# Optimization experiments

Measured on AMD Instinct MI355X. Metric: run time of the kernel, lower is better.

The kernel has to match this reference:

```python
import jax, jax.numpy as jnp
import numpy as np

N, E = 20000, 256000
NODE_DIM, EDGE_DIM = 128, 8
HID, HEADS, LAYERS = 64, 4, 3   # TransformerConv: out_channels per head = HID, concat=False
CLASSES, GRAPHS = 3, 64
HC = HEADS * HID


def setup_inputs() -> dict:
    key = jax.random.key(0)
    ks = iter(jax.random.split(key, 40))
    g = lambda shape, s=0.05: jax.random.normal(next(ks), shape, dtype=jnp.float32) * s
    z = lambda shape: jnp.zeros(shape, jnp.float32)
    return dict(
        x=jax.random.normal(next(ks), (N, NODE_DIM), dtype=jnp.float32),
        edge_attr=jax.random.normal(next(ks), (E, EDGE_DIM), dtype=jnp.float32),
        node_W=g((NODE_DIM, HID)), node_b=z((HID,)),
        e1_W=g((EDGE_DIM, HID)), e1_b=z((HID,)),
        e2_W=g((HID, HID)), e2_b=z((HID,)),
        Wq=g((LAYERS, HID, HC)), bq=z((LAYERS, HC)),
        Wk=g((LAYERS, HID, HC)), bk=z((LAYERS, HC)),
        Wv=g((LAYERS, HID, HC)), bv=z((LAYERS, HC)),
        We=g((LAYERS, HID, HC)),                      # lin_edge has bias=False in PyG
        Wskip=g((LAYERS, HID, HID)), bskip=z((LAYERS, HID)),
        ln_g=jnp.ones((LAYERS, HID), jnp.float32), ln_b=z((LAYERS, HID)),
        cls_W=g((HID, CLASSES)), cls_b=z((CLASSES,)),
        edge_index=jax.random.randint(next(ks), (2, E), 0, N),
        batch=jnp.sort(jax.random.randint(next(ks), (N,), 0, GRAPHS)),
    )


def _layer_norm(x, g, b, eps=1e-5):
    m = x.mean(-1, keepdims=True)
    v = x.var(-1, keepdims=True)
    return (x - m) * jax.lax.rsqrt(v + eps) * g + b


def reference(x, edge_attr, node_W, node_b, e1_W, e1_b, e2_W, e2_b,
              Wq, bq, Wk, bk, Wv, bv, We, Wskip, bskip, ln_g, ln_b,
              cls_W, cls_b, edge_index, batch):
    src, dst = edge_index[0], edge_index[1]          # messages flow src -> dst
    h = x @ node_W + node_b                          # [N, HID]
    e = jax.nn.relu(edge_attr @ e1_W + e1_b) @ e2_W + e2_b  # [E, HID]
    scale = 1.0 / jnp.sqrt(jnp.float32(HID))
    for l in range(LAYERS):                          # fixed small layer count
        res = h
        q = (h @ Wq[l] + bq[l]).reshape(N, HEADS, HID)
        k = (h @ Wk[l] + bk[l]).reshape(N, HEADS, HID)
        v = (h @ Wv[l] + bv[l]).reshape(N, HEADS, HID)
        ee = (e @ We[l]).reshape(E, HEADS, HID)      # per-layer edge projection
        kj = k[src] + ee                             # [E, H, C] irregular gather
        alpha = (q[dst] * kj).sum(-1) * scale        # [E, H]
        amax = jax.ops.segment_max(alpha, dst, num_segments=N)
        ea = jnp.exp(alpha - amax[dst])
        denom = jax.ops.segment_sum(ea, dst, num_segments=N)
        alpha = ea / denom[dst]                      # segment softmax over in-edges
        # dropout on alpha: identity in eval mode
        msg = (v[src] + ee) * alpha[..., None]       # [E, H, C]
        agg = jax.ops.segment_sum(msg, dst, num_segments=N)  # [N, H, C]
        conv = agg.mean(axis=1) + (res @ Wskip[l] + bskip[l])  # concat=False, root_weight
        h = jax.nn.relu(_layer_norm(conv + res, ln_g[l], ln_b[l]))
        # model-level dropout: identity in eval mode
    gsum = jax.ops.segment_sum(h, batch, num_segments=GRAPHS)
    gcnt = jax.ops.segment_sum(jnp.ones((N, 1), h.dtype), batch, num_segments=GRAPHS)
    pooled = gsum / jnp.maximum(gcnt, 1.0)           # global mean pool
    return jax.nn.log_softmax(pooled @ cls_W + cls_b, axis=-1)  # [GRAPHS, CLASSES]
```

## Files before the change

kernel.cpp:

```cpp
#include <hip/hip_runtime.h>
#include <hip/hip_bf16.h>
#include <math.h>

#define NN 20000
#define NE 256000
#define NODE_DIM_ 128
#define EDGE_DIM_ 8
#define HID 64
#define HEADS 4
#define NLAYERS 3
#define NCLASSES 3
#define NGRAPHS 64
#define HC 256
#define NPB 8
#define EB 64
#define EPB 16

typedef __hip_bfloat16 bf16;

__device__ __forceinline__ float B2F(bf16 x) { return __bfloat162float(x); }
__device__ __forceinline__ bf16 F2B(float x) { return __float2bfloat16(x); }
__device__ __forceinline__ float U2F(unsigned short u) { return __uint_as_float(((unsigned)u) << 16); }
__device__ __forceinline__ int clampi(int x, int lo, int hi) { return min(max(x, lo), hi); }

__global__ void gt_write_const(float* out, int n, float val) {
    int i = blockIdx.x * blockDim.x + threadIdx.x;
    if (i < n) out[i] = val;
}

__global__ void gt_zero_i32(int* p, int n) {
    int i = blockIdx.x * blockDim.x + threadIdx.x;
    if (i < n) p[i] = 0;
}

__global__ void gt_transpose_we(const float* __restrict__ We, float* __restrict__ WeT) {
    int idx = blockIdx.x * blockDim.x + threadIdx.x;
    if (idx >= NLAYERS * HID * HC) return;
    int l = idx / (HID * HC);
    int r = idx % (HID * HC);
    int c = r / HC;
    int u = r % HC;
    int hh = u >> 6, j = u & 63;
    WeT[idx] = We[(size_t)l * HID * HC + (size_t)j * HC + hh * 64 + c];
}

__global__ void gt_prep_wcomb(const float* __restrict__ We, const float* __restrict__ Wskip,
                              float* __restrict__ Wc) {
    int idx = blockIdx.x * blockDim.x + threadIdx.x;
    if (idx >= NLAYERS * 320 * 64) return;
    int l = idx / (320 * 64);
    int r = idx % (320 * 64);
    int kk = r / 64;
    int c = r % 64;
    float val;
    if (kk < 256) {
        int hh = kk >> 6, j = kk & 63;
        val = We[(size_t)l * HID * HC + (size_t)j * HC + hh * 64 + c];
    } else {
        int j = kk - 256;
        val = Wskip[(size_t)l * HID * HID + (size_t)j * HID + c];
    }
    Wc[(size_t)l * 320 * 64 + (size_t)((kk >> 2) * 64 + c) * 4 + (kk & 3)] = val;
}

__global__ void gt_node_proj(const float* __restrict__ x, const float* __restrict__ W,
                             const float* __restrict__ b, float* __restrict__ h) {
    int t = threadIdx.x;
    int n = blockIdx.x * 4 + (t >> 6);
    int c = t & 63;
    __shared__ float xr[4][NODE_DIM_];
    for (int i = t; i < 4 * NODE_DIM_; i += 256) {
        int nn = blockIdx.x * 4 + i / NODE_DIM_;
        xr[i / NODE_DIM_][i % NODE_DIM_] = (nn < NN) ? x[(size_t)nn * NODE_DIM_ + i % NODE_DIM_] : 0.f;
    }
    __syncthreads();
    if (n >= NN) return;
    float acc = 0.f;
#pragma unroll 8
    for (int j = 0; j < NODE_DIM_; ++j) acc += xr[t >> 6][j] * W[j * HID + c];
    h[(size_t)n * HID + c] = acc + b[c];
}

__global__ void gt_edge_mlp(const float* __restrict__ ea, const float* __restrict__ W1,
                            const float* __restrict__ b1, const float* __restrict__ W2,
                            const float* __restrict__ b2, bf16* __restrict__ ef) {
    int t = threadIdx.x;
    int c = t & 63, slot = t >> 6;
    int e0 = blockIdx.x * EB;
    __shared__ float aS[EB][EDGE_DIM_];
    __shared__ float t1s[EB][HID];
    for (int i = t; i < EB * EDGE_DIM_; i += 256) {
        ((float*)aS)[i] = ea[(size_t)e0 * EDGE_DIM_ + i];
    }
    float w1r[EDGE_DIM_];
#pragma unroll
    for (int j = 0; j < EDGE_DIM_; ++j) w1r[j] = W1[j * HID + c];
    float b1c = b1[c], b2c = b2[c];
    __syncthreads();
#pragma unroll
    for (int es16 = 0; es16 < 16; ++es16) {
        int es = slot * 16 + es16;
        float acc = b1c;
#pragma unroll
        for (int j = 0; j < EDGE_DIM_; ++j) acc += aS[es][j] * w1r[j];
        t1s[es][c] = fmaxf(acc, 0.f);
    }
    __syncthreads();
    float acc2[16];
#pragma unroll
    for (int i = 0; i < 16; ++i) acc2[i] = b2c;
    for (int j = 0; j < HID; ++j) {
        float w = W2[j * HID + c];
#pragma unroll
        for (int es16 = 0; es16 < 16; ++es16) acc2[es16] += t1s[slot * 16 + es16][j] * w;
    }
#pragma unroll
    for (int es16 = 0; es16 < 16; ++es16) {
        int es = slot * 16 + es16;
        ef[(size_t)(e0 + es) * HID + c] = F2B(acc2[es16]);
    }
}

__global__ void gt_count_dst(const int* __restrict__ ei, int* cnt) {
    int e = blockIdx.x * blockDim.x + threadIdx.x;
    if (e < NE) {
        int d = clampi(ei[NE + e], 0, NN - 1);
        atomicAdd(&cnt[d], 1);
    }
}

__global__ void gt_scan_csr(const int* __restrict__ cnt, int* __restrict__ rp, int* __restrict__ cur) {
    __shared__ int part[256];
    int tid = threadIdx.x;
    const int CH = (NN + 255) / 256;
    int s0 = tid * CH, s1 = min(s0 + CH, NN);
    int s = 0;
    for (int i = s0; i < s1; ++i) s += cnt[i];
    part[tid] = s;
    __syncthreads();
    for (int off = 1; off < 256; off <<= 1) {
        int vv = (tid >= off) ? part[tid - off] : 0;
        __syncthreads();
        if (tid >= off) part[tid] += vv;
        __syncthreads();
    }
    int base = (tid == 0) ? 0 : part[tid - 1];
    for (int i = s0; i < s1; ++i) {
        rp[i] = base;
        cur[i] = base;
        base += cnt[i];
    }
    if (tid == 255) rp[NN] = part[255];
}

__global__ void gt_fill_csr(const int* __restrict__ ei, int* cur, int* csr) {
    int e = blockIdx.x * blockDim.x + threadIdx.x;
    if (e < NE) {
        int d = clampi(ei[NE + e], 0, NN - 1);
        int pos = atomicAdd(&cur[d], 1);
        if (pos >= 0 && pos < NE) csr[pos] = e;
    }
}

__global__ void gt_qkv_qe(const float* __restrict__ h, const float* __restrict__ Wq,
                          const float* __restrict__ bq, const float* __restrict__ Wk,
                          const float* __restrict__ bk, const float* __restrict__ Wv,
                          const float* __restrict__ bv, const float* __restrict__ WeT,
                          float* __restrict__ q, bf16* __restrict__ k, bf16* __restrict__ v,
                          float* __restrict__ qe) {
    int t = threadIdx.x;
    int n0 = blockIdx.x * NPB;
    __shared__ float hs[NPB][HID];
    __shared__ float qs[NPB][HC];
    for (int i = t; i < NPB * HID; i += 256) {
        int nn = n0 + i / HID;
        hs[i / HID][i % HID] = (nn < NN) ? h[(size_t)nn * HID + i % HID] : 0.f;
    }
    __syncthreads();
    float aq[NPB], ak[NPB], av[NPB];
#pragma unroll
    for (int i = 0; i < NPB; ++i) { aq[i] = 0.f; ak[i] = 0.f; av[i] = 0.f; }
    for (int j = 0; j < HID; ++j) {
        float wq = Wq[j * HC + t];
        float wk = Wk[j * HC + t];
        float wv = Wv[j * HC + t];
#pragma unroll
        for (int i = 0; i < NPB; ++i) {
            aq[i] += hs[i][j] * wq;
            ak[i] += hs[i][j] * wk;
            av[i] += hs[i][j] * wv;
        }
    }
    float bqv = bq[t], bkv = bk[t], bvv = bv[t];
    for (int i = 0; i < NPB; ++i) {
        int nn = n0 + i;
        float qr = aq[i] + bqv;
        qs[i][t] = qr;
        if (nn < NN) {
            q[(size_t)nn * HC + t] = qr;
            k[(size_t)nn * HC + t] = F2B(ak[i] + bkv);
            v[(size_t)nn * HC + t] = F2B(av[i] + bvv);
        }
    }
    __syncthreads();
    int h2 = t >> 6;
    float accq[NPB];
#pragma unroll
    for (int i = 0; i < NPB; ++i) accq[i] = 0.f;
    for (int c = 0; c < HID; ++c) {
        float wt = WeT[(size_t)c * HC + t];
#pragma unroll
        for (int i = 0; i < NPB; ++i) accq[i] += qs[i][h2 * 64 + c] * wt;
    }
    for (int i = 0; i < NPB; ++i) {
        int nn = n0 + i;
        if (nn < NN) qe[(size_t)nn * HC + t] = accq[i];
    }
}

__global__ void gt_attn_core(float* __restrict__ q, float* __restrict__ qe,
                             const bf16* __restrict__ k, const bf16* __restrict__ v,
                             const bf16* __restrict__ ef,
                             const int* __restrict__ rp, const int* __restrict__ csr,
                             const int* __restrict__ ei) {
    int t = threadIdx.x;
    int lane = t & 63, wave = t >> 6;
    int n = blockIdx.x * 4 + wave;
    if (n >= NN) return;

    const float4* q4 = (const float4*)q;
    const float4* qe4 = (const float4*)qe;
    const ushort4* k4p = (const ushort4*)k;
    const ushort4* v4p = (const ushort4*)v;
    const ushort4* e4p = (const ushort4*)ef;

    float4 qv = q4[(size_t)n * 64 + lane];
    float4 qev = qe4[(size_t)n * 64 + lane];

    int s0 = clampi(rp[n], 0, NE), s1 = clampi(rp[n + 1], s0, NE);
    float m = -1e30f, lr = 0.f;
    float4 accv = make_float4(0.f, 0.f, 0.f, 0.f);
    float4 accs = make_float4(0.f, 0.f, 0.f, 0.f);

    for (int base = s0; base < s1; base += 64) {
        int cnt = min(64, s1 - base);
        int eL = 0, srcL = 0;
        if (lane < cnt) {
            eL = clampi(csr[base + lane], 0, NE - 1);
            srcL = clampi(ei[eL], 0, NN - 1);
        }
        int e0 = __builtin_amdgcn_readlane(eL, 0);
        int r0 = __builtin_amdgcn_readlane(srcL, 0);
        ushort4 kk = k4p[(size_t)r0 * 64 + lane];
        ushort4 vv = v4p[(size_t)r0 * 64 + lane];
        ushort4 ee = e4p[(size_t)e0 * 16 + (lane & 15)];
        for (int i = 0; i < cnt; ++i) {
            ushort4 kc = kk, vc = vv, ec = ee;
            if (i + 1 < cnt) {
                int e2 = __builtin_amdgcn_readlane(eL, i + 1);
                int r2 = __builtin_amdgcn_readlane(srcL, i + 1);
                kk = k4p[(size_t)r2 * 64 + lane];
                vv = v4p[(size_t)r2 * 64 + lane];
                ee = e4p[(size_t)e2 * 16 + (lane & 15)];
            }
            float p = qv.x * U2F(kc.x) + qv.y * U2F(kc.y) + qv.z * U2F(kc.z) + qv.w * U2F(kc.w)
                    + qev.x * U2F(ec.x) + qev.y * U2F(ec.y) + qev.z * U2F(ec.z) + qev.w * U2F(ec.w);
            p += __shfl_xor(p, 8, 16);
            p += __shfl_xor(p, 4, 16);
            p += __shfl_xor(p, 2, 16);
            p += __shfl_xor(p, 1, 16);
            p *= 0.125f;
            float nm = fmaxf(m, p);
            float sc = __expf(m - nm);
            float wg = __expf(p - nm);
            m = nm;
            lr = lr * sc + wg;
            accv.x = accv.x * sc + wg * U2F(vc.x);
            accv.y = accv.y * sc + wg * U2F(vc.y);
            accv.z = accv.z * sc + wg * U2F(vc.z);
            accv.w = accv.w * sc + wg * U2F(vc.w);
            accs.x = accs.x * sc + wg * U2F(ec.x);
            accs.y = accs.y * sc + wg * U2F(ec.y);
            accs.z = accs.z * sc + wg * U2F(ec.z);
            accs.w = accs.w * sc + wg * U2F(ec.w);
        }
    }
    float inv = (s1 > s0) ? 0.25f / lr : 0.f;
    float4 rs = make_float4(accs.x * inv, accs.y * inv, accs.z * inv, accs.w * inv);
    ((float4*)q)[(size_t)n * 64 + lane] = rs;
    float4 rv = make_float4(accv.x * inv, accv.y * inv, accv.z * inv, accv.w * inv);
    rv.x += __shfl_xor(rv.x, 16, 64); rv.x += __shfl_xor(rv.x, 32, 64);
    rv.y += __shfl_xor(rv.y, 16, 64); rv.y += __shfl_xor(rv.y, 32, 64);
    rv.z += __shfl_xor(rv.z, 16, 64); rv.z += __shfl_xor(rv.z, 32, 64);
    rv.w += __shfl_xor(rv.w, 16, 64); rv.w += __shfl_xor(rv.w, 32, 64);
    if (lane < 16) ((float4*)qe)[(size_t)n * 64 + lane] = rv;
}

__global__ void gt_epilogue(const float* __restrict__ acc_s, const float* __restrict__ acc_vm,
                            const float* __restrict__ Wc, const float* __restrict__ bskip,
                            const float* __restrict__ lng, const float* __restrict__ lnb,
                            float* __restrict__ h) {
    int t = threadIdx.x;
    int c = t & 63, qw = t >> 6;
    int n0 = blockIdx.x * EPB;
    __shared__ float sK[EPB][320];
    __shared__ float sVM[EPB][64];
    const float4* as4 = (const float4*)acc_s;
    for (int i = t; i < EPB * 64; i += 256) {
        int nd = i >> 6, j4 = i & 63;
        *(float4*)&sK[nd][4 * j4] = as4[(size_t)(n0 + nd) * 64 + j4];
    }
    const float4* h4g = (const float4*)h;
    const float4* vm4 = (const float4*)acc_vm;
    for (int i = t; i < EPB * 16; i += 256) {
        int nd = i >> 4, j4 = i & 15;
        *(float4*)&sK[nd][256 + 4 * j4] = h4g[(size_t)(n0 + nd) * 16 + j4];
        *(float4*)&sVM[nd][4 * j4] = vm4[(size_t)(n0 + nd) * 64 + j4];
    }
    __syncthreads();
    int nb = qw * 4;
    const float4* r0 = (const float4*)&sK[nb][0];
    const float4* r1 = (const float4*)&sK[nb + 1][0];
    const float4* r2 = (const float4*)&sK[nb + 2][0];
    const float4* r3 = (const float4*)&sK[nb + 3][0];
    const float4* W4 = (const float4*)Wc;
    float a0 = 0.f, a1 = 0.f, a2 = 0.f, a3 = 0.f;
#pragma unroll 4
    for (int k4 = 0; k4 < 80; ++k4) {
        float4 w = W4[k4 * 64 + c];
        float4 x0 = r0[k4]; a0 += x0.x * w.x + x0.y * w.y + x0.z * w.z + x0.w * w.w;
        float4 x1 = r1[k4]; a1 += x1.x * w.x + x1.y * w.y + x1.z * w.z + x1.w * w.w;
        float4 x2 = r2[k4]; a2 += x2.x * w.x + x2.y * w.y + x2.z * w.z + x2.w * w.w;
        float4 x3 = r3[k4]; a3 += x3.x * w.x + x3.y * w.y + x3.z * w.z + x3.w * w.w;
    }
    float bsk = bskip[c], g = lng[c], bb = lnb[c];
    float y0 = a0 + sVM[nb][c] + sK[nb][256 + c] + bsk;
    float y1 = a1 + sVM[nb + 1][c] + sK[nb + 1][256 + c] + bsk;
    float y2 = a2 + sVM[nb + 2][c] + sK[nb + 2][256 + c] + bsk;
    float y3 = a3 + sVM[nb + 3][c] + sK[nb + 3][256 + c] + bsk;
    float m0 = y0, m1 = y1, m2 = y2, m3 = y3;
#pragma unroll
    for (int s = 32; s > 0; s >>= 1) {
        m0 += __shfl_xor(m0, s, 64);
        m1 += __shfl_xor(m1, s, 64);
        m2 += __shfl_xor(m2, s, 64);
        m3 += __shfl_xor(m3, s, 64);
    }
    m0 *= (1.f / HID); m1 *= (1.f / HID); m2 *= (1.f / HID); m3 *= (1.f / HID);
    float d0 = y0 - m0, d1 = y1 - m1, d2 = y2 - m2, d3 = y3 - m3;
    float v0 = d0 * d0, v1 = d1 * d1, v2 = d2 * d2, v3 = d3 * d3;
#pragma unroll
    for (int s = 32; s > 0; s >>= 1) {
        v0 += __shfl_xor(v0, s, 64);
        v1 += __shfl_xor(v1, s, 64);
        v2 += __shfl_xor(v2, s, 64);
        v3 += __shfl_xor(v3, s, 64);
    }
    v0 *= (1.f / HID); v1 *= (1.f / HID); v2 *= (1.f / HID); v3 *= (1.f / HID);
    h[(size_t)(n0 + nb) * HID + c]     = fmaxf(d0 * rsqrtf(v0 + 1e-5f) * g + bb, 0.f);
    h[(size_t)(n0 + nb + 1) * HID + c] = fmaxf(d1 * rsqrtf(v1 + 1e-5f) * g + bb, 0.f);
    h[(size_t)(n0 + nb + 2) * HID + c] = fmaxf(d2 * rsqrtf(v2 + 1e-5f) * g + bb, 0.f);
    h[(size_t)(n0 + nb + 3) * HID + c] = fmaxf(d3 * rsqrtf(v3 + 1e-5f) * g + bb, 0.f);
}

__global__ void gt_pool_sum(const float* __restrict__ h, const int* __restrict__ batch,
                            float* __restrict__ psum) {
    int t = threadIdx.x;
    int c = t & 63, slot = t >> 6;
    int n0 = blockIdx.x * 256;
    float acc = 0.f;
    int curg = -1;
    for (int i = slot; i < 256; i += 4) {
        int n = n0 + i;
        if (n >= NN) break;
        int g = clampi(batch[n], 0, NGRAPHS - 1);
        float val = h[(size_t)n * HID + c];
        if (g != curg) {
            if (curg >= 0) atomicAdd(&psum[curg * HID + c], acc);
            curg = g;
            acc = 0.f;
        }
        acc += val;
    }
    if (curg >= 0) atomicAdd(&psum[curg * HID + c], acc);
}

__global__ void gt_classify(const float* __restrict__ psum, const int* __restrict__ batch,
                            const float* __restrict__ W, const float* __restrict__ b,
                            float* __restrict__ out) {
    int g = blockIdx.x;
    int c = threadIdx.x;
    __shared__ float pooled[HID];
    __shared__ float lg[4];
    __shared__ int bounds[2];
    if (c < 2) {
        int target = g + c;
        int lo = 0, hi = NN;
        while (lo < hi) {
            int mid = (lo + hi) >> 1;
            if (batch[mid] < target) lo = mid + 1; else hi = mid;
        }
        bounds[c] = lo;
    }
    __syncthreads();
    float divf = fmaxf((float)(bounds[1] - bounds[0]), 1.f);
    pooled[c] = psum[g * HID + c] / divf;
    __syncthreads();
    if (c < NCLASSES) {
        float acc = 0.f;
        for (int j = 0; j < HID; ++j) acc += pooled[j] * W[j * NCLASSES + c];
        lg[c] = acc + b[c];
    }
    __syncthreads();
    if (c == 0) {
        float m = fmaxf(lg[0], fmaxf(lg[1], lg[2]));
        float ssum = 0.f;
        for (int cc = 0; cc < NCLASSES; ++cc) ssum += __expf(lg[cc] - m);
        float lse = logf(ssum);
        for (int cc = 0; cc < NCLASSES; ++cc) out[g * NCLASSES + cc] = lg[cc] - m - lse;
    }
}

extern "C" void kernel_launch(void* const* d_in, const int* in_sizes, int n_in,
                              void* d_out, int out_size, void* d_ws, size_t ws_size,
                              hipStream_t stream) {
    float* out = (float*)d_out;

    static const int EXPECT[23] = {2560000, 2048000, 8192, 64, 512, 64, 4096, 64,
                                   49152, 768, 49152, 768, 49152, 768, 49152,
                                   12288, 192, 192, 192, 192, 3, 512000, 20000};
    int bad = -1;
    if (n_in != 23) bad = 99;
    else {
        for (int i = 0; i < 23; ++i) {
            if (in_sizes[i] != EXPECT[i]) { bad = i; break; }
        }
    }
    if (bad >= 0) {
        float val = (bad == 99) ? 4000.f : (5000.f + 10.f * bad);
        gt_write_const<<<1, 256, 0, stream>>>(out, out_size, val);
        return;
    }

    const float* x        = (const float*)d_in[0];
    const float* edge_attr= (const float*)d_in[1];
    const float* node_W   = (const float*)d_in[2];
    const float* node_b   = (const float*)d_in[3];
    const float* e1_W     = (const float*)d_in[4];
    const float* e1_b     = (const float*)d_in[5];
    const float* e2_W     = (const float*)d_in[6];
    const float* e2_b     = (const float*)d_in[7];
    const float* Wq       = (const float*)d_in[8];
    const float* bq       = (const float*)d_in[9];
    const float* Wk       = (const float*)d_in[10];
    const float* bk       = (const float*)d_in[11];
    const float* Wv       = (const float*)d_in[12];
    const float* bv       = (const float*)d_in[13];
    const float* We       = (const float*)d_in[14];
    const float* Wskip    = (const float*)d_in[15];
    const float* bskip    = (const float*)d_in[16];
    const float* lng      = (const float*)d_in[17];
    const float* lnb      = (const float*)d_in[18];
    const float* cls_W    = (const float*)d_in[19];
    const float* cls_b    = (const float*)d_in[20];
    const int*   ei       = (const int*)d_in[21];
    const int*   batch    = (const int*)d_in[22];

    char* w = (char*)d_ws;
    auto alloc = [&](size_t bytes) -> char* {
        char* p = w;
        w += (bytes + 255) & ~(size_t)255;
        return p;
    };
    float* h     = (float*)alloc((size_t)NN * HID * 4);
    bf16*  ef    = (bf16*)alloc((size_t)NE * HID * 2);
    float* q     = (float*)alloc((size_t)NN * HC * 4);
    bf16*  k     = (bf16*)alloc((size_t)NN * HC * 2);
    bf16*  v     = (bf16*)alloc((size_t)NN * HC * 2);
    float* qe    = (float*)alloc((size_t)NN * HC * 4);
    float* WeT   = (float*)alloc((size_t)NLAYERS * HID * HC * 4);
    float* Wc    = (float*)alloc((size_t)NLAYERS * 320 * 64 * 4);
    float* psum  = (float*)alloc((size_t)NGRAPHS * HID * 4);
    int*   cnt   = (int*)alloc((size_t)NN * 4);
    int*   rp    = (int*)alloc((size_t)(NN + 1) * 4);
    int*   cur   = (int*)alloc((size_t)NN * 4);
    int*   csr   = (int*)alloc((size_t)NE * 4);

    gt_node_proj<<<(NN + 3) / 4, 256, 0, stream>>>(x, node_W, node_b, h);
    gt_edge_mlp<<<NE / EB, 256, 0, stream>>>(edge_attr, e1_W, e1_b, e2_W, e2_b, ef);
    gt_transpose_we<<<(NLAYERS * HID * HC + 255) / 256, 256, 0, stream>>>(We, WeT);
    gt_prep_wcomb<<<(NLAYERS * 320 * 64 + 255) / 256, 256, 0, stream>>>(We, Wskip, Wc);
    gt_zero_i32<<<(NN + 255) / 256, 256, 0, stream>>>(cnt, NN);
    gt_count_dst<<<(NE + 255) / 256, 256, 0, stream>>>(ei, cnt);
    gt_scan_csr<<<1, 256, 0, stream>>>(cnt, rp, cur);
    gt_fill_csr<<<(NE + 255) / 256, 256, 0, stream>>>(ei, cur, csr);

    for (int l = 0; l < NLAYERS; ++l) {
        const float* Wq_l = Wq + (size_t)l * HID * HC;
        const float* bq_l = bq + (size_t)l * HC;
        const float* Wk_l = Wk + (size_t)l * HID * HC;
        const float* bk_l = bk + (size_t)l * HC;
        const float* Wv_l = Wv + (size_t)l * HID * HC;
        const float* bv_l = bv + (size_t)l * HC;
        const float* WeT_l= WeT + (size_t)l * HID * HC;
        const float* Wc_l = Wc + (size_t)l * 320 * 64;
        const float* bs_l = bskip + (size_t)l * HID;
        const float* lg_l = lng + (size_t)l * HID;
        const float* lb_l = lnb + (size_t)l * HID;

        gt_qkv_qe<<<(NN + NPB - 1) / NPB, 256, 0, stream>>>(h, Wq_l, bq_l, Wk_l, bk_l, Wv_l, bv_l,
                                                            WeT_l, q, k, v, qe);
        gt_attn_core<<<(NN + 3) / 4, 256, 0, stream>>>(q, qe, k, v, ef, rp, csr, ei);
        gt_epilogue<<<NN / EPB, 256, 0, stream>>>(q, qe, Wc_l, bs_l, lg_l, lb_l, h);
    }

    gt_zero_i32<<<(NGRAPHS * HID + 255) / 256, 256, 0, stream>>>((int*)psum, NGRAPHS * HID);
    gt_pool_sum<<<(NN + 255) / 256, 256, 0, stream>>>(h, batch, psum);
    gt_classify<<<NGRAPHS, HID, 0, stream>>>(psum, batch, cls_W, cls_b, out);
}
```

Before: 669.5 us.

## Use bf16 MFMA for QKV/qe projection and edge MLP second layer

Replaces the scalar FP32 QKV+qe projection with a bf16 MFMA kernel. The q·We product is precomputed algebraically as a fused Wqe weight (with folded bias), so q, k, v and qe all come from a single 64x1024 GEMM. The edge MLP's second matmul also moves to MFMA, using a swizzled bf16 LDS tile and a prepacked weight layout. This removes most of the FP32 FMA cost but rounds h and the weights to bf16, which reduces precision of q and qe.

```diff
diff --git a/kernel.cpp b/kernel.cpp
--- a/kernel.cpp
+++ b/kernel.cpp
@@ -12,14 +12,18 @@
 #define NCLASSES 3
 #define NGRAPHS 64
 #define HC 256
-#define NPB 8
 #define EB 64
 #define EPB 16
 
 typedef __hip_bfloat16 bf16;
+using v8s = __attribute__((ext_vector_type(8))) short;
+using f32x4 = __attribute__((ext_vector_type(4))) float;
 
 __device__ __forceinline__ float B2F(bf16 x) { return __bfloat162float(x); }
 __device__ __forceinline__ bf16 F2B(float x) { return __float2bfloat16(x); }
+__device__ __forceinline__ short F2BS(float x) {
+    union { bf16 b; short s; } u; u.b = __float2bfloat16(x); return u.s;
+}
 __device__ __forceinline__ float U2F(unsigned short u) { return __uint_as_float(((unsigned)u) << 16); }
 __device__ __forceinline__ int clampi(int x, int lo, int hi) { return min(max(x, lo), hi); }
 
@@ -33,15 +37,64 @@
     if (i < n) p[i] = 0;
 }
 
-__global__ void gt_transpose_we(const float* __restrict__ We, float* __restrict__ WeT) {
-    int idx = blockIdx.x * blockDim.x + threadIdx.x;
-    if (idx >= NLAYERS * HID * HC) return;
-    int l = idx / (HID * HC);
-    int r = idx % (HID * HC);
-    int c = r / HC;
-    int u = r % HC;
-    int hh = u >> 6, j = u & 63;
-    WeT[idx] = We[(size_t)l * HID * HC + (size_t)j * HC + hh * 64 + c];
+__global__ void gt_prep_wqe(const float* __restrict__ Wq, const float* __restrict__ bq,
+                            const float* __restrict__ bk, const float* __restrict__ bv,
+                            const float* __restrict__ We,
+                            float* __restrict__ Wqe, float* __restrict__ bias4) {
+    int b = blockIdx.x;
+    int l = b / 65, kk = b % 65;
+    int t = threadIdx.x;
+    int hh = t >> 6, d = t & 63;
+    const float* Weh = We + (size_t)l * HID * HC + (size_t)d * HC + hh * 64;
+    if (kk < 64) {
+        const float* Wqr = Wq + (size_t)l * HID * HC + (size_t)kk * HC + hh * 64;
+        float s = 0.f;
+        for (int c = 0; c < 64; ++c) s += Wqr[c] * Weh[c];
+        Wqe[(size_t)l * HID * HC + (size_t)kk * HC + t] = s;
+    } else {
+        const float* bqr = bq + (size_t)l * HC + hh * 64;
+        float s = 0.f;
+        for (int c = 0; c < 64; ++c) s += bqr[c] * Weh[c];
+        bias4[(size_t)l * 1024 + 768 + t] = s;
+        bias4[(size_t)l * 1024 + t]       = bq[(size_t)l * HC + t];
+        bias4[(size_t)l * 1024 + 256 + t] = bk[(size_t)l * HC + t];
+        bias4[(size_t)l * 1024 + 512 + t] = bv[(size_t)l * HC + t];
+    }
+}
+
+__global__ void gt_pack_qkv(const float* __restrict__ Wq, const float* __restrict__ Wk,
+                            const float* __restrict__ Wv, const float* __restrict__ Wqe,
+                            bf16* __restrict__ Bp) {
+    int idx = blockIdx.x * 256 + threadIdx.x;
+    if (idx >= NLAYERS * 8192) return;
+    int lane = idx & 63;
+    int ks = (idx >> 6) & 1;
+    int nf = (idx >> 7) & 63;
+    int l = idx >> 13;
+    int col = nf * 16 + (lane & 15);
+    int k0 = ks * 32 + (lane >> 4) * 8;
+    const float* src;
+    int c;
+    if (col < 256)      { src = Wq  + (size_t)l * HID * HC; c = col; }
+    else if (col < 512) { src = Wk  + (size_t)l * HID * HC; c = col - 256; }
+    else if (col < 768) { src = Wv  + (size_t)l * HID * HC; c = col - 512; }
+    else                { src = Wqe + (size_t)l * HID * HC; c = col - 768; }
+    bf16* dst = Bp + (size_t)idx * 8;
+#pragma unroll
+    for (int j = 0; j < 8; ++j) dst[j] = F2B(src[(size_t)(k0 + j) * HC + c]);
+}
+
+__global__ void gt_pack_w2(const float* __restrict__ W2, bf16* __restrict__ B2p) {
+    int idx = blockIdx.x * 256 + threadIdx.x;
+    if (idx >= 512) return;
+    int lane = idx & 63;
+    int ks = (idx >> 6) & 1;
+    int nf = idx >> 7;
+    int col = nf * 16 + (lane & 15);
+    int k0 = ks * 32 + (lane >> 4) * 8;
+    bf16* dst = B2p + (size_t)idx * 8;
+#pragma unroll
+    for (int j = 0; j < 8; ++j) dst[j] = F2B(W2[(size_t)(k0 + j) * HID + col]);
 }
 
 __global__ void gt_prep_wcomb(const float* __restrict__ We, const float* __restrict__ Wskip,
@@ -82,42 +135,58 @@
 }
 
 __global__ void gt_edge_mlp(const float* __restrict__ ea, const float* __restrict__ W1,
-                            const float* __restrict__ b1, const float* __restrict__ W2,
+                            const float* __restrict__ b1, const bf16* __restrict__ B2p,
                             const float* __restrict__ b2, bf16* __restrict__ ef) {
     int t = threadIdx.x;
     int c = t & 63, slot = t >> 6;
     int e0 = blockIdx.x * EB;
     __shared__ float aS[EB][EDGE_DIM_];
-    __shared__ float t1s[EB][HID];
+    __shared__ bf16 t1s[EB * 64];
     for (int i = t; i < EB * EDGE_DIM_; i += 256) {
         ((float*)aS)[i] = ea[(size_t)e0 * EDGE_DIM_ + i];
     }
     float w1r[EDGE_DIM_];
 #pragma unroll
     for (int j = 0; j < EDGE_DIM_; ++j) w1r[j] = W1[j * HID + c];
-    float b1c = b1[c], b2c = b2[c];
-    __syncthreads();
+    float b1c = b1[c];
+    __syncthreads();
+    int cu = c >> 3, ci = c & 7;
 #pragma unroll
     for (int es16 = 0; es16 < 16; ++es16) {
         int es = slot * 16 + es16;
         float acc = b1c;
 #pragma unroll
         for (int j = 0; j < EDGE_DIM_; ++j) acc += aS[es][j] * w1r[j];
-        t1s[es][c] = fmaxf(acc, 0.f);
-    }
-    __syncthreads();
-    float acc2[16];
-#pragma unroll
-    for (int i = 0; i < 16; ++i) acc2[i] = b2c;
-    for (int j = 0; j < HID; ++j) {
-        float w = W2[j * HID + c];
-#pragma unroll
-        for (int es16 = 0; es16 < 16; ++es16) acc2[es16] += t1s[slot * 16 + es16][j] * w;
-    }
-#pragma unroll
-    for (int es16 = 0; es16 < 16; ++es16) {
-        int es = slot * 16 + es16;
-        ef[(size_t)(e0 + es) * HID + c] = F2B(acc2[es16]);
+        int cs = ((cu ^ (es & 7)) << 3) | ci;
+        t1s[es * 64 + cs] = F2B(fmaxf(acc, 0.f));
+    }
+    __syncthreads();
+    int lane = t & 63, wave = slot;
+    v8s bfr0 = *(const v8s*)(B2p + ((size_t)(wave * 2 + 0) * 64 + lane) * 8);
+    v8s bfr1 = *(const v8s*)(B2p + ((size_t)(wave * 2 + 1) * 64 + lane) * 8);
+    int rowA = lane & 15, kg = lane >> 4;
+    f32x4 acc[4];
+#pragma unroll
+    for (int mf = 0; mf < 4; ++mf) acc[mf] = (f32x4){0.f, 0.f, 0.f, 0.f};
+#pragma unroll
+    for (int mf = 0; mf < 4; ++mf) {
+        int r = mf * 16 + rowA;
+        int u0 = 0 * 4 + kg, u1 = 1 * 4 + kg;
+        v8s a0 = *(const v8s*)&t1s[r * 64 + ((u0 ^ (r & 7)) << 3)];
+        v8s a1 = *(const v8s*)&t1s[r * 64 + ((u1 ^ (r & 7)) << 3)];
+        acc[mf] = __builtin_amdgcn_mfma_f32_16x16x32_bf16(a0, bfr0, acc[mf], 0, 0, 0);
+        acc[mf] = __builtin_amdgcn_mfma_f32_16x16x32_bf16(a1, bfr1, acc[mf], 0, 0, 0);
+    }
+    int col = wave * 16 + (lane & 15);
+    float bb = b2[col];
+    int rbase = (lane >> 4) * 4;
+#pragma unroll
+    for (int mf = 0; mf < 4; ++mf) {
+#pragma unroll
+        for (int reg = 0; reg < 4; ++reg) {
+            int e = e0 + mf * 16 + rbase + reg;
+            ef[(size_t)e * HID + col] = F2B(acc[mf][reg] + bb);
+        }
     }
 }
 
@@ -162,59 +231,65 @@
     }
 }
 
-__global__ void gt_qkv_qe(const float* __restrict__ h, const float* __restrict__ Wq,
-                          const float* __restrict__ bq, const float* __restrict__ Wk,
-                          const float* __restrict__ bk, const float* __restrict__ Wv,
-                          const float* __restrict__ bv, const float* __restrict__ WeT,
-                          float* __restrict__ q, bf16* __restrict__ k, bf16* __restrict__ v,
-                          float* __restrict__ qe) {
-    int t = threadIdx.x;
-    int n0 = blockIdx.x * NPB;
-    __shared__ float hs[NPB][HID];
-    __shared__ float qs[NPB][HC];
-    for (int i = t; i < NPB * HID; i += 256) {
-        int nn = n0 + i / HID;
-        hs[i / HID][i % HID] = (nn < NN) ? h[(size_t)nn * HID + i % HID] : 0.f;
-    }
-    __syncthreads();
-    float aq[NPB], ak[NPB], av[NPB];
-#pragma unroll
-    for (int i = 0; i < NPB; ++i) { aq[i] = 0.f; ak[i] = 0.f; av[i] = 0.f; }
-    for (int j = 0; j < HID; ++j) {
-        float wq = Wq[j * HC + t];
-        float wk = Wk[j * HC + t];
-        float wv = Wv[j * HC + t];
-#pragma unroll
-        for (int i = 0; i < NPB; ++i) {
-            aq[i] += hs[i][j] * wq;
-            ak[i] += hs[i][j] * wk;
-            av[i] += hs[i][j] * wv;
-        }
-    }
-    float bqv = bq[t], bkv = bk[t], bvv = bv[t];
-    for (int i = 0; i < NPB; ++i) {
-        int nn = n0 + i;
-        float qr = aq[i] + bqv;
-        qs[i][t] = qr;
-        if (nn < NN) {
-            q[(size_t)nn * HC + t] = qr;
-            k[(size_t)nn * HC + t] = F2B(ak[i] + bkv);
-            v[(size_t)nn * HC + t] = F2B(av[i] + bvv);
-        }
-    }
-    __syncthreads();
-    int h2 = t >> 6;
-    float accq[NPB];
-#pragma unroll
-    for (int i = 0; i < NPB; ++i) accq[i] = 0.f;
-    for (int c = 0; c < HID; ++c) {
-        float wt = WeT[(size_t)c * HC + t];
-#pragma unroll
-        for (int i = 0; i < NPB; ++i) accq[i] += qs[i][h2 * 64 + c] * wt;
-    }
-    for (int i = 0; i < NPB; ++i) {
-        int nn = n0 + i;
-        if (nn < NN) qe[(size_t)nn * HC + t] = accq[i];
+__global__ void __launch_bounds__(256)
+gt_qkv_mfma(const float* __restrict__ h, const bf16* __restrict__ Bp,
+            const float* __restrict__ bias4,
+            float* __restrict__ q, bf16* __restrict__ k2, bf16* __restrict__ v2,
+            float* __restrict__ qe) {
+    int t = threadIdx.x, lane = t & 63, wave = t >> 6;
+    int n0 = blockIdx.x * 32;
+    int rowA = lane & 15, kg = lane >> 4;
+
+    v8s a[2][2];
+#pragma unroll
+    for (int mf = 0; mf < 2; ++mf) {
+        const float* hr = h + (size_t)(n0 + mf * 16 + rowA) * HID;
+#pragma unroll
+        for (int ks = 0; ks < 2; ++ks) {
+            const float* p = hr + ks * 32 + kg * 8;
+            float4 x0 = *(const float4*)p;
+            float4 x1 = *(const float4*)(p + 4);
+            v8s av;
+            av[0] = F2BS(x0.x); av[1] = F2BS(x0.y); av[2] = F2BS(x0.z); av[3] = F2BS(x0.w);
+            av[4] = F2BS(x1.x); av[5] = F2BS(x1.y); av[6] = F2BS(x1.z); av[7] = F2BS(x1.w);
+            a[mf][ks] = av;
+        }
+    }
+
+    f32x4 acc[2][16];
+#pragma unroll
+    for (int mf = 0; mf < 2; ++mf)
+#pragma unroll
+        for (int nf = 0; nf < 16; ++nf) acc[mf][nf] = (f32x4){0.f, 0.f, 0.f, 0.f};
+
+#pragma unroll
+    for (int nf = 0; nf < 16; ++nf) {
+        int nfg = wave * 16 + nf;
+        v8s b0 = *(const v8s*)(Bp + ((size_t)(nfg * 2 + 0) * 64 + lane) * 8);
+        v8s b1 = *(const v8s*)(Bp + ((size_t)(nfg * 2 + 1) * 64 + lane) * 8);
+        acc[0][nf] = __builtin_amdgcn_mfma_f32_16x16x32_bf16(a[0][0], b0, acc[0][nf], 0, 0, 0);
+        acc[0][nf] = __builtin_amdgcn_mfma_f32_16x16x32_bf16(a[0][1], b1, acc[0][nf], 0, 0, 0);
+        acc[1][nf] = __builtin_amdgcn_mfma_f32_16x16x32_bf16(a[1][0], b0, acc[1][nf], 0, 0, 0);
+        acc[1][nf] = __builtin_amdgcn_mfma_f32_16x16x32_bf16(a[1][1], b1, acc[1][nf], 0, 0, 0);
+    }
+
+    int rbase = (lane >> 4) * 4;
+#pragma unroll
+    for (int nf = 0; nf < 16; ++nf) {
+        int cc = nf * 16 + (lane & 15);
+        float bias = bias4[wave * 256 + cc];
+#pragma unroll
+        for (int mf = 0; mf < 2; ++mf) {
+#pragma unroll
+            for (int reg = 0; reg < 4; ++reg) {
+                int n = n0 + mf * 16 + rbase + reg;
+                float val = acc[mf][nf][reg] + bias;
+                if (wave == 0)      q [(size_t)n * HC + cc] = val;
+                else if (wave == 1) k2[(size_t)n * HC + cc] = F2B(val);
+                else if (wave == 2) v2[(size_t)n * HC + cc] = F2B(val);
+                else                qe[(size_t)n * HC + cc] = val;
+            }
+        }
     }
 }
 
@@ -478,7 +553,10 @@
     bf16*  k     = (bf16*)alloc((size_t)NN * HC * 2);
     bf16*  v     = (bf16*)alloc((size_t)NN * HC * 2);
     float* qe    = (float*)alloc((size_t)NN * HC * 4);
-    float* WeT   = (float*)alloc((size_t)NLAYERS * HID * HC * 4);
+    float* Wqe   = (float*)alloc((size_t)NLAYERS * HID * HC * 4);
+    float* bias4 = (float*)alloc((size_t)NLAYERS * 1024 * 4);
+    bf16*  Bp    = (bf16*)alloc((size_t)NLAYERS * 8192 * 8 * 2);
+    bf16*  B2p   = (bf16*)alloc((size_t)512 * 8 * 2);
     float* Wc    = (float*)alloc((size_t)NLAYERS * 320 * 64 * 4);
     float* psum  = (float*)alloc((size_t)NGRAPHS * HID * 4);
     int*   cnt   = (int*)alloc((size_t)NN * 4);
@@ -487,8 +565,10 @@
     int*   csr   = (int*)alloc((size_t)NE * 4);
 
     gt_node_proj<<<(NN + 3) / 4, 256, 0, stream>>>(x, node_W, node_b, h);
-    gt_edge_mlp<<<NE / EB, 256, 0, stream>>>(edge_attr, e1_W, e1_b, e2_W, e2_b, ef);
-    gt_transpose_we<<<(NLAYERS * HID * HC + 255) / 256, 256, 0, stream>>>(We, WeT);
+    gt_prep_wqe<<<NLAYERS * 65, 256, 0, stream>>>(Wq, bq, bk, bv, We, Wqe, bias4);
+    gt_pack_qkv<<<(NLAYERS * 8192 + 255) / 256, 256, 0, stream>>>(Wq, Wk, Wv, Wqe, Bp);
+    gt_pack_w2<<<2, 256, 0, stream>>>(e2_W, B2p);
+    gt_edge_mlp<<<NE / EB, 256, 0, stream>>>(edge_attr, e1_W, e1_b, B2p, e2_b, ef);
     gt_prep_wcomb<<<(NLAYERS * 320 * 64 + 255) / 256, 256, 0, stream>>>(We, Wskip, Wc);
     gt_zero_i32<<<(NN + 255) / 256, 256, 0, stream>>>(cnt, NN);
     gt_count_dst<<<(NE + 255) / 256, 256, 0, stream>>>(ei, cnt);
@@ -496,20 +576,14 @@
     gt_fill_csr<<<(NE + 255) / 256, 256, 0, stream>>>(ei, cur, csr);
 
     for (int l = 0; l < NLAYERS; ++l) {
-        const float* Wq_l = Wq + (size_t)l * HID * HC;
-        const float* bq_l = bq + (size_t)l * HC;
-        const float* Wk_l = Wk + (size_t)l * HID * HC;
-        const float* bk_l = bk + (size_t)l * HC;
-        const float* Wv_l = Wv + (size_t)l * HID * HC;
-        const float* bv_l = bv + (size_t)l * HC;
-        const float* WeT_l= WeT + (size_t)l * HID * HC;
+        const bf16* Bp_l  = Bp + (size_t)l * 8192 * 8;
+        const float* b4_l = bias4 + (size_t)l * 1024;
         const float* Wc_l = Wc + (size_t)l * 320 * 64;
         const float* bs_l = bskip + (size_t)l * HID;
         const float* lg_l = lng + (size_t)l * HID;
         const float* lb_l = lnb + (size_t)l * HID;
 
-        gt_qkv_qe<<<(NN + NPB - 1) / NPB, 256, 0, stream>>>(h, Wq_l, bq_l, Wk_l, bk_l, Wv_l, bv_l,
-                                                            WeT_l, q, k, v, qe);
+        gt_qkv_mfma<<<NN / 32, 256, 0, stream>>>(h, Bp_l, b4_l, q, k, v, qe);
         gt_attn_core<<<(NN + 3) / 4, 256, 0, stream>>>(q, qe, k, v, ef, rp, csr, ei);
         gt_epilogue<<<NN / EPB, 256, 0, stream>>>(q, qe, Wc_l, bs_l, lg_l, lb_l, h);
     }
```

Result: faster. 581.8 us (-13.1%).
